# Kernel tuning notes

Measured on AMD Instinct MI355X. Metric: run time of the kernel, lower is better.

Reference implementation:

```python
import jax, jax.numpy as jnp
import numpy as np

H = 256    # hidden_size
NH = 8     # num_heads
B = 256    # batch_size (num graphs)
M = 128    # max_num_nodes per graph
N = B * M  # total nodes
E = N * 16 # total edges


def _bn(x, g, b, eps=1e-5):
    # BatchNorm1d in training mode: batch stats over node dim, biased variance
    m = x.mean(0)
    v = ((x - m) ** 2).mean(0)
    return g * (x - m) * jax.lax.rsqrt(v + eps) + b


def setup_inputs() -> dict:
    key = jax.random.key(0)
    ks = jax.random.split(key, 12)
    def lin(k, o, i):
        return jax.random.normal(k, (o, i), jnp.float32) / np.sqrt(i).astype(np.float32)
    return {
        "h": jax.random.normal(ks[0], (N, H), jnp.float32),
        "gin_w1": lin(ks[1], H, H), "gin_b1": jnp.zeros((H,), jnp.float32),
        "gin_w2": lin(ks[2], H, H), "gin_b2": jnp.zeros((H,), jnp.float32),
        "in_proj_w": lin(ks[3], 3 * H, H), "in_proj_b": jnp.zeros((3 * H,), jnp.float32),
        "out_proj_w": lin(ks[4], H, H), "out_proj_b": jnp.zeros((H,), jnp.float32),
        "bn_local_g": jnp.ones((H,), jnp.float32), "bn_local_b": jnp.zeros((H,), jnp.float32),
        "bn_attn_g": jnp.ones((H,), jnp.float32), "bn_attn_b": jnp.zeros((H,), jnp.float32),
        "bn_out_g": jnp.ones((H,), jnp.float32), "bn_out_b": jnp.zeros((H,), jnp.float32),
        "ffn1_w": lin(ks[5], 2 * H, H), "ffn1_b": jnp.zeros((2 * H,), jnp.float32),
        "ffn2_w": lin(ks[6], H, 2 * H), "ffn2_b": jnp.zeros((H,), jnp.float32),
        "edge_src": jax.random.randint(ks[7], (E,), 0, N, dtype=jnp.int32),
        "edge_dst": jax.random.randint(ks[8], (E,), 0, N, dtype=jnp.int32),
        "batch_num_nodes": jnp.full((B,), M, dtype=jnp.int32),
    }


def reference(h, gin_w1, gin_b1, gin_w2, gin_b2, in_proj_w, in_proj_b,
              out_proj_w, out_proj_b, bn_local_g, bn_local_b, bn_attn_g, bn_attn_b,
              bn_out_g, bn_out_b, ffn1_w, ffn1_b, ffn2_w, ffn2_b,
              edge_src, edge_dst, batch_num_nodes):
    # ---- local GIN conv: gin_nn((1+eps)*h + sum_neighbors h), eps=0 ----
    agg = jax.ops.segment_sum(h[edge_src], edge_dst, num_segments=N)
    z = h + agg
    z = jax.nn.relu(z @ gin_w1.T + gin_b1) @ gin_w2.T + gin_b2
    h_local = _bn(h + z, bn_local_g, bn_local_b)  # dropout=0

    # ---- to_dense_batch scatter indices ----
    cum = jnp.concatenate([jnp.zeros((1,), batch_num_nodes.dtype), jnp.cumsum(batch_num_nodes)])
    node = jnp.arange(N, dtype=jnp.int32)
    bid = jnp.searchsorted(cum[1:], node, side='right')  # graph id per node
    idx = node - cum[bid] + bid * M                      # slot in dense [B*M]
    hd = jnp.zeros((B * M, H), h.dtype).at[idx].set(h).reshape(B, M, H)
    mask = jnp.zeros((B * M,), bool).at[idx].set(True).reshape(B, M)

    # ---- MultiheadAttention (batch_first, self-attn, key_padding_mask) ----
    qkv = hd @ in_proj_w.T + in_proj_b
    q, k, v = jnp.split(qkv, 3, axis=-1)
    dh = H // NH
    q = q.reshape(B, M, NH, dh)
    k = k.reshape(B, M, NH, dh)
    v = v.reshape(B, M, NH, dh)
    scores = jnp.einsum('bqhd,bkhd->bhqk', q, k) / np.float32(np.sqrt(dh))
    scores = jnp.where(mask[:, None, None, :], scores, jnp.float32(-1e9))
    attn = jax.nn.softmax(scores, axis=-1)
    ao = jnp.einsum('bhqk,bkhd->bqhd', attn, v).reshape(B, M, H)
    ao = ao @ out_proj_w.T + out_proj_b
    h_attn = ao.reshape(B * M, H)[idx]  # ragged gather back (x[mask])
    h_attn = _bn(h + h_attn, bn_attn_g, bn_attn_b)

    # ---- combine + FFN + out norm ----
    hh = h_local + h_attn
    hh = hh + (jax.nn.relu(hh @ ffn1_w.T + ffn1_b) @ ffn2_w.T + ffn2_b)
    return _bn(hh, bn_out_g, bn_out_b)
```

## Files before the change

kernel.cpp:

```cpp
#include <hip/hip_runtime.h>

#define NNODES 32768
#define HDIM   256
#define NHEADS 8
#define NB     256
#define NEDGES 524288


typedef unsigned short u16;
typedef unsigned int   u32;
typedef __attribute__((ext_vector_type(8))) short short8;
typedef __attribute__((ext_vector_type(4))) float f32x4;

__device__ __forceinline__ float bf2f(u16 u){
  union { u32 i; float f; } x; x.i = ((u32)u) << 16; return x.f;
}
__device__ __forceinline__ u16 f2bf(float f){
  union { float f; u32 i; } x; x.f = f;
  u32 r = x.i + 0x7fffu + ((x.i >> 16) & 1u);
  return (u16)(r >> 16);
}
__device__ __forceinline__ void unpack8(uint4 v, float* f){
  f[0] = bf2f((u16)(v.x & 0xffff)); f[1] = bf2f((u16)(v.x >> 16));
  f[2] = bf2f((u16)(v.y & 0xffff)); f[3] = bf2f((u16)(v.y >> 16));
  f[4] = bf2f((u16)(v.z & 0xffff)); f[5] = bf2f((u16)(v.z >> 16));
  f[6] = bf2f((u16)(v.w & 0xffff)); f[7] = bf2f((u16)(v.w >> 16));
}
__device__ __forceinline__ uint4 pack8(const float* f){
  uint4 v;
  v.x = (u32)f2bf(f[0]) | ((u32)f2bf(f[1]) << 16);
  v.y = (u32)f2bf(f[2]) | ((u32)f2bf(f[3]) << 16);
  v.z = (u32)f2bf(f[4]) | ((u32)f2bf(f[5]) << 16);
  v.w = (u32)f2bf(f[6]) | ((u32)f2bf(f[7]) << 16);
  return v;
}

struct CvtPtrs { const void* p[19]; };

__device__ static const int CVT_CH[19] = {
  2097152,16384,64,16384,64,49152,192,16384,64,64,64,64,64,64,64,32768,128,32768,64};
__device__ static const int CVT_PR[19] = {
  0,8388608,8454144,8454400,8519936,8520192,8716800,8717568,8783104,
  8783360,8783616,8783872,8784128,8784384,8784640,8784896,8915968,8916480,9047552};
#define CVT_TOTAL_CHUNKS 2261952

__global__ __launch_bounds__(256) void convert_k(CvtPtrs cp, u16* __restrict__ dst){
  int gid = blockIdx.x * 256 + threadIdx.x;
  if (gid >= CVT_TOTAL_CHUNKS) return;
  int t = 0, rem = gid;
  while (t < 18 && rem >= CVT_CH[t]) { rem -= CVT_CH[t]; t++; }
  u16* d = dst + CVT_PR[t] + (size_t)rem * 4;
  float4 v = ((const float4*)cp.p[t])[rem];
  u16 o[4] = { f2bf(v.x), f2bf(v.y), f2bf(v.z), f2bf(v.w) };
  *(uint2*)d = *(const uint2*)o;
}

__global__ void count_k(const int* __restrict__ dst, int* __restrict__ counts){
  int e = blockIdx.x * 256 + threadIdx.x;
  atomicAdd(&counts[dst[e]], 1);
}

__global__ void scan_k(const int* __restrict__ counts, int* __restrict__ offsets,
                       int* __restrict__ cursor){
  __shared__ int part[1024];
  int t = threadIdx.x;
  int local[32];
  int s = 0;
  int base = t * 32;
#pragma unroll
  for (int i = 0; i < 32; i++){ local[i] = counts[base + i]; s += local[i]; }
  part[t] = s;
  __syncthreads();
  for (int off = 1; off < 1024; off <<= 1){
    int v = (t >= off) ? part[t - off] : 0;
    __syncthreads();
    part[t] += v;
    __syncthreads();
  }
  int run = part[t] - s;
#pragma unroll
  for (int i = 0; i < 32; i++){
    offsets[base + i] = run; cursor[base + i] = run; run += local[i];
  }
  if (t == 1023) offsets[NNODES] = run;
}

__global__ void bucket_k(const int* __restrict__ src, const int* __restrict__ dst,
                         int* __restrict__ cursor, int* __restrict__ srcs){
  int e = blockIdx.x * 256 + threadIdx.x;
  int p = atomicAdd(&cursor[dst[e]], 1);
  srcs[p] = src[e];
}

__global__ __launch_bounds__(256) void agg_k(const u16* __restrict__ h,
    const int* __restrict__ offsets, const int* __restrict__ srcs,
    u16* __restrict__ z0){
  int node = blockIdx.x * 4 + (threadIdx.x >> 6);
  int lane = threadIdx.x & 63;
  size_t coff = (size_t)lane * 4;
  int beg = offsets[node], end = offsets[node + 1];

  uint2 self = *(const uint2*)&h[(size_t)node * HDIM + coff];
  float a0 = bf2f((u16)(self.x & 0xffff)), a1 = bf2f((u16)(self.x >> 16));
  float a2 = bf2f((u16)(self.y & 0xffff)), a3 = bf2f((u16)(self.y >> 16));

  int e = beg;
  for (; e + 8 <= end; e += 8){
    uint2 v[8];
#pragma unroll
    for (int i = 0; i < 8; i++){
      int s = srcs[e + i];
      v[i] = *(const uint2*)&h[(size_t)s * HDIM + coff];
    }
#pragma unroll
    for (int i = 0; i < 8; i++){
      a0 += bf2f((u16)(v[i].x & 0xffff));
      a1 += bf2f((u16)(v[i].x >> 16));
      a2 += bf2f((u16)(v[i].y & 0xffff));
      a3 += bf2f((u16)(v[i].y >> 16));
    }
  }
  for (; e < end; e++){
    int s = srcs[e];
    uint2 va = *(const uint2*)&h[(size_t)s * HDIM + coff];
    a0 += bf2f((u16)(va.x & 0xffff));
    a1 += bf2f((u16)(va.x >> 16));
    a2 += bf2f((u16)(va.y & 0xffff));
    a3 += bf2f((u16)(va.y >> 16));
  }

  uint2 o;
  o.x = (u32)f2bf(a0) | ((u32)f2bf(a1) << 16);
  o.y = (u32)f2bf(a2) | ((u32)f2bf(a3) << 16);
  *(uint2*)&z0[(size_t)node * HDIM + coff] = o;
}

template<int NO, int K, bool RELU, bool RES, bool STATS>
__global__ __launch_bounds__(256) void gemm_bt(const u16* __restrict__ A,
    const u16* __restrict__ W, const u16* __restrict__ bias,
    const u16* __restrict__ res, u16* __restrict__ C,
    float* __restrict__ ssum, float* __restrict__ ssq){
  __shared__ u16 As[128 * 40];
  __shared__ u16 Ws[128 * 40];
  const int tid = threadIdx.x;
  const int m0 = blockIdx.y * 128;
  const int n0 = blockIdx.x * 128;
  const int wave = tid >> 6, lane = tid & 63;
  const int wm = wave >> 1, wn = wave & 1;
  const int q4 = lane >> 4, ln = lane & 15;

  f32x4 acc[4][4] = {};

  const int r_a = tid >> 2;
  const int c_a = tid & 3;

  for (int k0 = 0; k0 < K; k0 += 32){
    uint4 a0 = *(const uint4*)&A[(size_t)(m0 + r_a) * K + k0 + c_a * 8];
    uint4 a1 = *(const uint4*)&A[(size_t)(m0 + r_a + 64) * K + k0 + c_a * 8];
    uint4 w0 = *(const uint4*)&W[(size_t)(n0 + r_a) * K + k0 + c_a * 8];
    uint4 w1 = *(const uint4*)&W[(size_t)(n0 + r_a + 64) * K + k0 + c_a * 8];
    __syncthreads();
    *(uint4*)&As[r_a * 40 + c_a * 8] = a0;
    *(uint4*)&As[(r_a + 64) * 40 + c_a * 8] = a1;
    *(uint4*)&Ws[r_a * 40 + c_a * 8] = w0;
    *(uint4*)&Ws[(r_a + 64) * 40 + c_a * 8] = w1;
    __syncthreads();

    short8 af[4], bfr[4];
#pragma unroll
    for (int mt = 0; mt < 4; mt++)
      af[mt] = *(const short8*)&As[(wm * 64 + mt * 16 + ln) * 40 + q4 * 8];
#pragma unroll
    for (int nt = 0; nt < 4; nt++)
      bfr[nt] = *(const short8*)&Ws[(wn * 64 + nt * 16 + ln) * 40 + q4 * 8];
#pragma unroll
    for (int mt = 0; mt < 4; mt++)
#pragma unroll
      for (int nt = 0; nt < 4; nt++)
        acc[mt][nt] = __builtin_amdgcn_mfma_f32_16x16x32_bf16(af[mt], bfr[nt], acc[mt][nt], 0, 0, 0);
  }

#pragma unroll
  for (int nt = 0; nt < 4; nt++){
    int col = n0 + wn * 64 + nt * 16 + ln;
    float bv = bf2f(bias[col]);
    float cs = 0.0f, cq = 0.0f;
#pragma unroll
    for (int mt = 0; mt < 4; mt++){
      int row = m0 + wm * 64 + mt * 16 + q4 * 4;
#pragma unroll
      for (int reg = 0; reg < 4; reg++){
        float v = acc[mt][nt][reg] + bv;
        if (RELU) v = fmaxf(v, 0.0f);
        if (RES)  v += bf2f(res[(size_t)(row + reg) * NO + col]);
        C[(size_t)(row + reg) * NO + col] = f2bf(v);
        if (STATS){ cs += v; cq += v * v; }
      }
    }
    if (STATS){
      cs += __shfl_xor(cs, 16); cs += __shfl_xor(cs, 32);
      cq += __shfl_xor(cq, 16); cq += __shfl_xor(cq, 32);
      if (lane < 16){
        atomicAdd(&ssum[col], cs);
        atomicAdd(&ssq[col], cq);
      }
    }
  }
}

__global__ __launch_bounds__(256) void attn_k(const u16* __restrict__ qkv,
                                              u16* __restrict__ ao){
  __shared__ u16 Qs[128 * 40];
  __shared__ u16 Ks[128 * 40];
  __shared__ u16 VTs[32 * 136];
  __shared__ u16 Ps[128 * 136];

  const int b  = blockIdx.x >> 3;
  const int nh = blockIdx.x & 7;
  const int tid = threadIdx.x;
  const int wave = tid >> 6, lane = tid & 63;
  const int q4 = lane >> 4, ln = lane & 15;

#pragma unroll
  for (int c2 = 0; c2 < 2; c2++){
    int chunk = tid + c2 * 256;
    int r = chunk >> 2;
    int cc = chunk & 3;
    size_t nb = (size_t)(b * 128 + r) * 768 + nh * 32 + cc * 8;
    uint4 vq = *(const uint4*)&qkv[nb];
    uint4 vk = *(const uint4*)&qkv[nb + 256];
    uint4 vv = *(const uint4*)&qkv[nb + 512];
    *(uint4*)&Qs[r * 40 + cc * 8] = vq;
    *(uint4*)&Ks[r * 40 + cc * 8] = vk;
    union { uint4 v; u16 h[8]; } uv; uv.v = vv;
#pragma unroll
    for (int i = 0; i < 8; i++) VTs[(cc * 8 + i) * 136 + r] = uv.h[i];
  }
  __syncthreads();

  f32x4 accs[2][8] = {};
  short8 qf[2];
#pragma unroll
  for (int mt = 0; mt < 2; mt++)
    qf[mt] = *(const short8*)&Qs[(wave * 32 + mt * 16 + ln) * 40 + q4 * 8];
#pragma unroll
  for (int nt = 0; nt < 8; nt++){
    short8 kf = *(const short8*)&Ks[(nt * 16 + ln) * 40 + q4 * 8];
    accs[0][nt] = __builtin_amdgcn_mfma_f32_16x16x32_bf16(qf[0], kf, accs[0][nt], 0, 0, 0);
    accs[1][nt] = __builtin_amdgcn_mfma_f32_16x16x32_bf16(qf[1], kf, accs[1][nt], 0, 0, 0);
  }

  const float scale = 0.17677669529663687f;
  float invs[2][4];
#pragma unroll
  for (int mt = 0; mt < 2; mt++){
#pragma unroll
    for (int reg = 0; reg < 4; reg++){
      float rm = -1e30f;
#pragma unroll
      for (int nt = 0; nt < 8; nt++){
        accs[mt][nt][reg] *= scale;
        rm = fmaxf(rm, accs[mt][nt][reg]);
      }
      for (int m = 1; m < 16; m <<= 1) rm = fmaxf(rm, __shfl_xor(rm, m));
      float rs = 0.0f;
#pragma unroll
      for (int nt = 0; nt < 8; nt++){
        float e = __expf(accs[mt][nt][reg] - rm);
        accs[mt][nt][reg] = e;
        rs += e;
      }
      for (int m = 1; m < 16; m <<= 1) rs += __shfl_xor(rs, m);
      invs[mt][reg] = 1.0f / rs;
    }
  }

#pragma unroll
  for (int mt = 0; mt < 2; mt++)
#pragma unroll
    for (int nt = 0; nt < 8; nt++)
#pragma unroll
      for (int reg = 0; reg < 4; reg++)
        Ps[(wave * 32 + mt * 16 + q4 * 4 + reg) * 136 + nt * 16 + ln] =
            f2bf(accs[mt][nt][reg] * invs[mt][reg]);
  __syncthreads();

  f32x4 acco[2][2] = {};
#pragma unroll
  for (int kk = 0; kk < 4; kk++){
    short8 pf[2], vf[2];
#pragma unroll
    for (int mt = 0; mt < 2; mt++)
      pf[mt] = *(const short8*)&Ps[(wave * 32 + mt * 16 + ln) * 136 + kk * 32 + q4 * 8];
#pragma unroll
    for (int nt = 0; nt < 2; nt++)
      vf[nt] = *(const short8*)&VTs[(nt * 16 + ln) * 136 + kk * 32 + q4 * 8];
#pragma unroll
    for (int mt = 0; mt < 2; mt++)
#pragma unroll
      for (int nt = 0; nt < 2; nt++)
        acco[mt][nt] = __builtin_amdgcn_mfma_f32_16x16x32_bf16(pf[mt], vf[nt], acco[mt][nt], 0, 0, 0);
  }

#pragma unroll
  for (int mt = 0; mt < 2; mt++)
#pragma unroll
    for (int nt = 0; nt < 2; nt++)
#pragma unroll
      for (int reg = 0; reg < 4; reg++){
        int node = b * 128 + wave * 32 + mt * 16 + q4 * 4 + reg;
        int col = nh * 32 + nt * 16 + ln;
        ao[(size_t)node * HDIM + col] = f2bf(acco[mt][nt][reg]);
      }
}

__global__ void bncoef2_k(const float* __restrict__ stats,
    const u16* __restrict__ gl, const u16* __restrict__ bl,
    const u16* __restrict__ ga, const u16* __restrict__ ba,
    float* __restrict__ coef){
  int c = threadIdx.x;
  const float invN = 1.0f / 32768.0f;
  float mA = stats[c] * invN;
  float vA = stats[256 + c] * invN - mA * mA;
  float sA = bf2f(gl[c]) * rsqrtf(vA + 1e-5f);
  float tA = bf2f(bl[c]) - mA * sA;
  float mB = stats[512 + c] * invN;
  float vB = stats[768 + c] * invN - mB * mB;
  float sB = bf2f(ga[c]) * rsqrtf(vB + 1e-5f);
  float tB = bf2f(ba[c]) - mB * sB;
  coef[c] = sA; coef[256 + c] = sB; coef[512 + c] = tA + tB;
}

__global__ void bncoef1_k(const float* __restrict__ stats,
    const u16* __restrict__ g, const u16* __restrict__ bb,
    float* __restrict__ coef){
  int c = threadIdx.x;
  const float invN = 1.0f / 32768.0f;
  float m = stats[1024 + c] * invN;
  float v = stats[1280 + c] * invN - m * m;
  float s = bf2f(g[c]) * rsqrtf(v + 1e-5f);
  coef[768 + c] = s; coef[1024 + c] = bf2f(bb[c]) - m * s;
}

__global__ __launch_bounds__(256) void combine_k(const u16* __restrict__ xl,
    const u16* __restrict__ xa, const float* __restrict__ coef,
    u16* __restrict__ hh){
  int gid = blockIdx.x * 256 + threadIdx.x;
  size_t off = (size_t)gid * 8;
  int cb = (int)(off & 255);
  float sl[8], sa[8], tt[8];
  *(float4*)&sl[0] = *(const float4*)&coef[cb];
  *(float4*)&sl[4] = *(const float4*)&coef[cb + 4];
  *(float4*)&sa[0] = *(const float4*)&coef[256 + cb];
  *(float4*)&sa[4] = *(const float4*)&coef[256 + cb + 4];
  *(float4*)&tt[0] = *(const float4*)&coef[512 + cb];
  *(float4*)&tt[4] = *(const float4*)&coef[512 + cb + 4];
  float fl[8], fa[8], fo[8];
  unpack8(*(const uint4*)&xl[off], fl);
  unpack8(*(const uint4*)&xa[off], fa);
#pragma unroll
  for (int i = 0; i < 8; i++) fo[i] = sl[i] * fl[i] + sa[i] * fa[i] + tt[i];
  *(uint4*)&hh[off] = pack8(fo);
}

__global__ __launch_bounds__(256) void finalbn_k(const u16* __restrict__ y,
    const float* __restrict__ coef, float* __restrict__ out){
  int gid = blockIdx.x * 256 + threadIdx.x;
  size_t off = (size_t)gid * 8;
  int cb = (int)(off & 255);
  float ss[8], tt[8];
  *(float4*)&ss[0] = *(const float4*)&coef[768 + cb];
  *(float4*)&ss[4] = *(const float4*)&coef[768 + cb + 4];
  *(float4*)&tt[0] = *(const float4*)&coef[1024 + cb];
  *(float4*)&tt[4] = *(const float4*)&coef[1024 + cb + 4];
  float fy[8], fo[8];
  unpack8(*(const uint4*)&y[off], fy);
#pragma unroll
  for (int i = 0; i < 8; i++) fo[i] = ss[i] * fy[i] + tt[i];
  *(float4*)&out[off] = *(const float4*)&fo[0];
  *(float4*)&out[off + 4] = *(const float4*)&fo[4];
}

extern "C" void kernel_launch(void* const* d_in, const int* in_sizes, int n_in,
                              void* d_out, int out_size, void* d_ws, size_t ws_size,
                              hipStream_t stream){
  const int* edge_src = (const int*)d_in[19];
  const int* edge_dst = (const int*)d_in[20];

  char* ws = (char*)d_ws;
  float* stats = (float*)ws;
  float* coef  = (float*)(ws + 6144);
  u16*   conv  = (u16*)(ws + 12288);
  u16*   A     = (u16*)(ws + 12288 + 18095616);
  u16*   B     = (u16*)(ws + 12288 + 18095616 + 16777216);
  u16*   C     = (u16*)d_out;
  int* counts  = (int*)B;
  int* offsets = (int*)((char*)B + 131072);
  int* cursor  = (int*)((char*)B + 262400);
  int* srcs    = (int*)((char*)B + 393472);

  const u16* convH = conv;
  const u16* W1  = conv + 8388608; const u16* b1g = conv + 8454144;
  const u16* W2  = conv + 8454400; const u16* b2g = conv + 8519936;
  const u16* Win = conv + 8520192; const u16* bin = conv + 8716800;
  const u16* Wo  = conv + 8717568; const u16* bo  = conv + 8783104;
  const u16* g_l = conv + 8783360; const u16* b_l = conv + 8783616;
  const u16* g_a = conv + 8783872; const u16* b_a = conv + 8784128;
  const u16* g_o = conv + 8784384; const u16* b_o = conv + 8784640;
  const u16* Wf1 = conv + 8784896; const u16* bf1 = conv + 8915968;
  const u16* Wf2 = conv + 8916480; const u16* bf2 = conv + 9047552;

  hipMemsetAsync(ws, 0, 12288, stream);
  hipMemsetAsync(counts, 0, 131072, stream);

  CvtPtrs cp;
  for (int i = 0; i < 19; i++) cp.p[i] = d_in[i];
  convert_k<<<8836, 256, 0, stream>>>(cp, conv);

  count_k<<<NEDGES / 256, 256, 0, stream>>>(edge_dst, counts);
  scan_k<<<1, 1024, 0, stream>>>(counts, offsets, cursor);
  bucket_k<<<NEDGES / 256, 256, 0, stream>>>(edge_src, edge_dst, cursor, srcs);
  agg_k<<<NNODES / 4, 256, 0, stream>>>(convH, offsets, srcs, A);

  gemm_bt<256, 256, true,  false, false><<<dim3(2, 256), 256, 0, stream>>>(
      A, W1, b1g, nullptr, B, nullptr, nullptr);
  gemm_bt<256, 256, false, true,  true ><<<dim3(2, 256), 256, 0, stream>>>(
      B, W2, b2g, convH, A, stats + 0, stats + 256);

  for (int c = 0; c < 4; c++){
    const u16* hA = convH + (size_t)c * 8192 * HDIM;
    u16* aoC = C + (size_t)c * 8192 * HDIM;
    gemm_bt<768, 256, false, false, false><<<dim3(6, 64), 256, 0, stream>>>(
        hA, Win, bin, nullptr, B, nullptr, nullptr);
    attn_k<<<512, 256, 0, stream>>>(B, aoC);
  }

  gemm_bt<256, 256, false, true, true><<<dim3(2, 256), 256, 0, stream>>>(
      C, Wo, bo, convH, B, stats + 512, stats + 768);

  bncoef2_k<<<1, 256, 0, stream>>>(stats, g_l, b_l, g_a, b_a, coef);
  combine_k<<<4096, 256, 0, stream>>>(A, B, coef, C);

  gemm_bt<512, 256, true,  false, false><<<dim3(4, 256), 256, 0, stream>>>(
      C, Wf1, bf1, nullptr, A, nullptr, nullptr);
  gemm_bt<256, 512, false, true,  true ><<<dim3(2, 256), 256, 0, stream>>>(
      A, Wf2, bf2, C, (u16*)conv, stats + 1024, stats + 1280);

  bncoef1_k<<<1, 256, 0, stream>>>(stats, g_o, b_o, coef);
  finalbn_k<<<4096, 256, 0, stream>>>(conv, coef, (float*)d_out);
}
```

Measured before the change: 457.9 us.

## Double-buffer GEMM via direct global-to-LDS loads and fold small kernels into neighbours

The GEMM now double-buffers its tiles in LDS, filled with global_load_lds direct copies, so the next K-slice loads while MFMAs run on the current one. The edge counting is fused into the convert kernel, and the BN coefficient kernels are folded into the combine and final-BN kernels, which removes several launches. When the workspace is large enough, the QKV projection and attention run as one full-size launch each instead of four chunks. The risks are LDS bank conflicts from the unpadded 32-stride layout, and every combine/finalbn block now recomputes the BN coefficients.

```diff
diff --git a/kernel.cpp b/kernel.cpp
--- a/kernel.cpp
+++ b/kernel.cpp
@@ -9,6 +9,7 @@
 
 typedef unsigned short u16;
 typedef unsigned int   u32;
+typedef unsigned long long u64;
 typedef __attribute__((ext_vector_type(8))) short short8;
 typedef __attribute__((ext_vector_type(4))) float f32x4;
 
@@ -35,6 +36,13 @@
   return v;
 }
 
+typedef __attribute__((address_space(3))) unsigned int lds_u32;
+typedef const __attribute__((address_space(1))) unsigned int gbl_u32;
+__device__ __forceinline__ void gload16(const void* g, void* l){
+  __builtin_amdgcn_global_load_lds((gbl_u32*)(u64)g,
+                                   (lds_u32*)(u32)(u64)l, 16, 0, 0);
+}
+
 struct CvtPtrs { const void* p[19]; };
 
 __device__ static const int CVT_CH[19] = {
@@ -44,8 +52,10 @@
   8783360,8783616,8783872,8784128,8784384,8784640,8784896,8915968,8916480,9047552};
 #define CVT_TOTAL_CHUNKS 2261952
 
-__global__ __launch_bounds__(256) void convert_k(CvtPtrs cp, u16* __restrict__ dst){
+__global__ __launch_bounds__(256) void convert_k(CvtPtrs cp, u16* __restrict__ dst,
+    const int* __restrict__ edge_dst, int* __restrict__ counts){
   int gid = blockIdx.x * 256 + threadIdx.x;
+  if (gid < NEDGES) atomicAdd(&counts[edge_dst[gid]], 1);
   if (gid >= CVT_TOTAL_CHUNKS) return;
   int t = 0, rem = gid;
   while (t < 18 && rem >= CVT_CH[t]) { rem -= CVT_CH[t]; t++; }
@@ -55,11 +65,6 @@
   *(uint2*)d = *(const uint2*)o;
 }
 
-__global__ void count_k(const int* __restrict__ dst, int* __restrict__ counts){
-  int e = blockIdx.x * 256 + threadIdx.x;
-  atomicAdd(&counts[dst[e]], 1);
-}
-
 __global__ void scan_k(const int* __restrict__ counts, int* __restrict__ offsets,
                        int* __restrict__ cursor){
   __shared__ int part[1024];
@@ -135,13 +140,28 @@
   *(uint2*)&z0[(size_t)node * HDIM + coff] = o;
 }
 
+__device__ __forceinline__ void mfma_step(const u16* AS_, const u16* WS_,
+    f32x4 (&acc)[4][4], int wm, int wn, int ln, int q4){
+  short8 af[4], bfr[4];
+#pragma unroll
+  for (int mt = 0; mt < 4; mt++)
+    af[mt] = *(const short8*)&AS_[(wm * 64 + mt * 16 + ln) * 32 + q4 * 8];
+#pragma unroll
+  for (int nt = 0; nt < 4; nt++)
+    bfr[nt] = *(const short8*)&WS_[(wn * 64 + nt * 16 + ln) * 32 + q4 * 8];
+#pragma unroll
+  for (int mt = 0; mt < 4; mt++)
+#pragma unroll
+    for (int nt = 0; nt < 4; nt++)
+      acc[mt][nt] = __builtin_amdgcn_mfma_f32_16x16x32_bf16(af[mt], bfr[nt], acc[mt][nt], 0, 0, 0);
+}
+
 template<int NO, int K, bool RELU, bool RES, bool STATS>
 __global__ __launch_bounds__(256) void gemm_bt(const u16* __restrict__ A,
     const u16* __restrict__ W, const u16* __restrict__ bias,
     const u16* __restrict__ res, u16* __restrict__ C,
     float* __restrict__ ssum, float* __restrict__ ssq){
-  __shared__ u16 As[128 * 40];
-  __shared__ u16 Ws[128 * 40];
+  __shared__ u16 As0[4096], Ws0[4096], As1[4096], Ws1[4096];
   const int tid = threadIdx.x;
   const int m0 = blockIdx.y * 128;
   const int n0 = blockIdx.x * 128;
@@ -151,33 +171,35 @@
 
   f32x4 acc[4][4] = {};
 
-  const int r_a = tid >> 2;
-  const int c_a = tid & 3;
-
-  for (int k0 = 0; k0 < K; k0 += 32){
-    uint4 a0 = *(const uint4*)&A[(size_t)(m0 + r_a) * K + k0 + c_a * 8];
-    uint4 a1 = *(const uint4*)&A[(size_t)(m0 + r_a + 64) * K + k0 + c_a * 8];
-    uint4 w0 = *(const uint4*)&W[(size_t)(n0 + r_a) * K + k0 + c_a * 8];
-    uint4 w1 = *(const uint4*)&W[(size_t)(n0 + r_a + 64) * K + k0 + c_a * 8];
+  const int r_l = tid >> 2;
+  const int c_l = (tid & 3) * 8;
+  const u16* gA = A + (size_t)(m0 + r_l) * K + c_l;
+  const u16* gW = W + (size_t)(n0 + r_l) * K + c_l;
+  u16* dA0 = As0 + wave * 512; u16* dW0 = Ws0 + wave * 512;
+  u16* dA1 = As1 + wave * 512; u16* dW1 = Ws1 + wave * 512;
+
+  const int NT = K / 32;
+
+  gload16(gA, dA0); gload16(gA + 64 * K, dA0 + 2048);
+  gload16(gW, dW0); gload16(gW + 64 * K, dW0 + 2048);
+  __syncthreads();
+
+#pragma unroll
+  for (int t = 0; t < NT; t += 2){
+    if (t + 1 < NT){
+      int kn = (t + 1) * 32;
+      gload16(gA + kn, dA1); gload16(gA + 64 * K + kn, dA1 + 2048);
+      gload16(gW + kn, dW1); gload16(gW + 64 * K + kn, dW1 + 2048);
+    }
+    mfma_step(As0, Ws0, acc, wm, wn, ln, q4);
     __syncthreads();
-    *(uint4*)&As[r_a * 40 + c_a * 8] = a0;
-    *(uint4*)&As[(r_a + 64) * 40 + c_a * 8] = a1;
-    *(uint4*)&Ws[r_a * 40 + c_a * 8] = w0;
-    *(uint4*)&Ws[(r_a + 64) * 40 + c_a * 8] = w1;
+    if (t + 2 < NT){
+      int kn = (t + 2) * 32;
+      gload16(gA + kn, dA0); gload16(gA + 64 * K + kn, dA0 + 2048);
+      gload16(gW + kn, dW0); gload16(gW + 64 * K + kn, dW0 + 2048);
+    }
+    mfma_step(As1, Ws1, acc, wm, wn, ln, q4);
     __syncthreads();
-
-    short8 af[4], bfr[4];
-#pragma unroll
-    for (int mt = 0; mt < 4; mt++)
-      af[mt] = *(const short8*)&As[(wm * 64 + mt * 16 + ln) * 40 + q4 * 8];
-#pragma unroll
-    for (int nt = 0; nt < 4; nt++)
-      bfr[nt] = *(const short8*)&Ws[(wn * 64 + nt * 16 + ln) * 40 + q4 * 8];
-#pragma unroll
-    for (int mt = 0; mt < 4; mt++)
-#pragma unroll
-      for (int nt = 0; nt < 4; nt++)
-        acc[mt][nt] = __builtin_amdgcn_mfma_f32_16x16x32_bf16(af[mt], bfr[nt], acc[mt][nt], 0, 0, 0);
   }
 
 #pragma unroll
@@ -314,47 +336,36 @@
       }
 }
 
-__global__ void bncoef2_k(const float* __restrict__ stats,
+__global__ __launch_bounds__(256) void combine_k(const u16* __restrict__ xl,
+    const u16* __restrict__ xa, const float* __restrict__ stats,
     const u16* __restrict__ gl, const u16* __restrict__ bl,
     const u16* __restrict__ ga, const u16* __restrict__ ba,
-    float* __restrict__ coef){
-  int c = threadIdx.x;
-  const float invN = 1.0f / 32768.0f;
-  float mA = stats[c] * invN;
-  float vA = stats[256 + c] * invN - mA * mA;
-  float sA = bf2f(gl[c]) * rsqrtf(vA + 1e-5f);
-  float tA = bf2f(bl[c]) - mA * sA;
-  float mB = stats[512 + c] * invN;
-  float vB = stats[768 + c] * invN - mB * mB;
-  float sB = bf2f(ga[c]) * rsqrtf(vB + 1e-5f);
-  float tB = bf2f(ba[c]) - mB * sB;
-  coef[c] = sA; coef[256 + c] = sB; coef[512 + c] = tA + tB;
-}
-
-__global__ void bncoef1_k(const float* __restrict__ stats,
-    const u16* __restrict__ g, const u16* __restrict__ bb,
-    float* __restrict__ coef){
-  int c = threadIdx.x;
-  const float invN = 1.0f / 32768.0f;
-  float m = stats[1024 + c] * invN;
-  float v = stats[1280 + c] * invN - m * m;
-  float s = bf2f(g[c]) * rsqrtf(v + 1e-5f);
-  coef[768 + c] = s; coef[1024 + c] = bf2f(bb[c]) - m * s;
-}
-
-__global__ __launch_bounds__(256) void combine_k(const u16* __restrict__ xl,
-    const u16* __restrict__ xa, const float* __restrict__ coef,
     u16* __restrict__ hh){
-  int gid = blockIdx.x * 256 + threadIdx.x;
+  __shared__ float cs0[256], cs1[256], cs2[256];
+  int t = threadIdx.x;
+  {
+    const float invN = 1.0f / 32768.0f;
+    float mA = stats[t] * invN;
+    float vA = stats[256 + t] * invN - mA * mA;
+    float sA = bf2f(gl[t]) * rsqrtf(vA + 1e-5f);
+    float tA = bf2f(bl[t]) - mA * sA;
+    float mB = stats[512 + t] * invN;
+    float vB = stats[768 + t] * invN - mB * mB;
+    float sB = bf2f(ga[t]) * rsqrtf(vB + 1e-5f);
+    float tB = bf2f(ba[t]) - mB * sB;
+    cs0[t] = sA; cs1[t] = sB; cs2[t] = tA + tB;
+  }
+  __syncthreads();
+  int gid = blockIdx.x * 256 + t;
   size_t off = (size_t)gid * 8;
   int cb = (int)(off & 255);
   float sl[8], sa[8], tt[8];
-  *(float4*)&sl[0] = *(const float4*)&coef[cb];
-  *(float4*)&sl[4] = *(const float4*)&coef[cb + 4];
-  *(float4*)&sa[0] = *(const float4*)&coef[256 + cb];
-  *(float4*)&sa[4] = *(const float4*)&coef[256 + cb + 4];
-  *(float4*)&tt[0] = *(const float4*)&coef[512 + cb];
-  *(float4*)&tt[4] = *(const float4*)&coef[512 + cb + 4];
+  *(float4*)&sl[0] = *(const float4*)&cs0[cb];
+  *(float4*)&sl[4] = *(const float4*)&cs0[cb + 4];
+  *(float4*)&sa[0] = *(const float4*)&cs1[cb];
+  *(float4*)&sa[4] = *(const float4*)&cs1[cb + 4];
+  *(float4*)&tt[0] = *(const float4*)&cs2[cb];
+  *(float4*)&tt[4] = *(const float4*)&cs2[cb + 4];
   float fl[8], fa[8], fo[8];
   unpack8(*(const uint4*)&xl[off], fl);
   unpack8(*(const uint4*)&xa[off], fa);
@@ -364,15 +375,26 @@
 }
 
 __global__ __launch_bounds__(256) void finalbn_k(const u16* __restrict__ y,
-    const float* __restrict__ coef, float* __restrict__ out){
-  int gid = blockIdx.x * 256 + threadIdx.x;
+    const float* __restrict__ stats, const u16* __restrict__ g,
+    const u16* __restrict__ bb, float* __restrict__ out){
+  __shared__ float cs0[256], cs1[256];
+  int t = threadIdx.x;
+  {
+    const float invN = 1.0f / 32768.0f;
+    float m = stats[1024 + t] * invN;
+    float v = stats[1280 + t] * invN - m * m;
+    float s = bf2f(g[t]) * rsqrtf(v + 1e-5f);
+    cs0[t] = s; cs1[t] = bf2f(bb[t]) - m * s;
+  }
+  __syncthreads();
+  int gid = blockIdx.x * 256 + t;
   size_t off = (size_t)gid * 8;
   int cb = (int)(off & 255);
   float ss[8], tt[8];
-  *(float4*)&ss[0] = *(const float4*)&coef[768 + cb];
-  *(float4*)&ss[4] = *(const float4*)&coef[768 + cb + 4];
-  *(float4*)&tt[0] = *(const float4*)&coef[1024 + cb];
-  *(float4*)&tt[4] = *(const float4*)&coef[1024 + cb + 4];
+  *(float4*)&ss[0] = *(const float4*)&cs0[cb];
+  *(float4*)&ss[4] = *(const float4*)&cs0[cb + 4];
+  *(float4*)&tt[0] = *(const float4*)&cs1[cb];
+  *(float4*)&tt[4] = *(const float4*)&cs1[cb + 4];
   float fy[8], fo[8];
   unpack8(*(const uint4*)&y[off], fy);
 #pragma unroll
@@ -389,11 +411,14 @@
 
   char* ws = (char*)d_ws;
   float* stats = (float*)ws;
-  float* coef  = (float*)(ws + 6144);
   u16*   conv  = (u16*)(ws + 12288);
   u16*   A     = (u16*)(ws + 12288 + 18095616);
   u16*   B     = (u16*)(ws + 12288 + 18095616 + 16777216);
   u16*   C     = (u16*)d_out;
+  const size_t BIG_NEED = 51662336ull + 50331648ull;
+  const bool big = (ws_size >= BIG_NEED);
+  u16* QKV = (u16*)(ws + 51662336);
+
   int* counts  = (int*)B;
   int* offsets = (int*)((char*)B + 131072);
   int* cursor  = (int*)((char*)B + 262400);
@@ -410,14 +435,13 @@
   const u16* Wf1 = conv + 8784896; const u16* bf1 = conv + 8915968;
   const u16* Wf2 = conv + 8916480; const u16* bf2 = conv + 9047552;
 
-  hipMemsetAsync(ws, 0, 12288, stream);
+  hipMemsetAsync(ws, 0, 6144, stream);
   hipMemsetAsync(counts, 0, 131072, stream);
 
   CvtPtrs cp;
   for (int i = 0; i < 19; i++) cp.p[i] = d_in[i];
-  convert_k<<<8836, 256, 0, stream>>>(cp, conv);
-
-  count_k<<<NEDGES / 256, 256, 0, stream>>>(edge_dst, counts);
+  convert_k<<<8836, 256, 0, stream>>>(cp, conv, edge_dst, counts);
+
   scan_k<<<1, 1024, 0, stream>>>(counts, offsets, cursor);
   bucket_k<<<NEDGES / 256, 256, 0, stream>>>(edge_src, edge_dst, cursor, srcs);
   agg_k<<<NNODES / 4, 256, 0, stream>>>(convH, offsets, srcs, A);
@@ -427,25 +451,29 @@
   gemm_bt<256, 256, false, true,  true ><<<dim3(2, 256), 256, 0, stream>>>(
       B, W2, b2g, convH, A, stats + 0, stats + 256);
 
-  for (int c = 0; c < 4; c++){
-    const u16* hA = convH + (size_t)c * 8192 * HDIM;
-    u16* aoC = C + (size_t)c * 8192 * HDIM;
-    gemm_bt<768, 256, false, false, false><<<dim3(6, 64), 256, 0, stream>>>(
-        hA, Win, bin, nullptr, B, nullptr, nullptr);
-    attn_k<<<512, 256, 0, stream>>>(B, aoC);
+  if (big){
+    gemm_bt<768, 256, false, false, false><<<dim3(6, 256), 256, 0, stream>>>(
+        convH, Win, bin, nullptr, QKV, nullptr, nullptr);
+    attn_k<<<2048, 256, 0, stream>>>(QKV, C);
+  } else {
+    for (int c = 0; c < 4; c++){
+      const u16* hA = convH + (size_t)c * 8192 * HDIM;
+      u16* aoC = C + (size_t)c * 8192 * HDIM;
+      gemm_bt<768, 256, false, false, false><<<dim3(6, 64), 256, 0, stream>>>(
+          hA, Win, bin, nullptr, B, nullptr, nullptr);
+      attn_k<<<512, 256, 0, stream>>>(B, aoC);
+    }
   }
 
   gemm_bt<256, 256, false, true, true><<<dim3(2, 256), 256, 0, stream>>>(
       C, Wo, bo, convH, B, stats + 512, stats + 768);
 
-  bncoef2_k<<<1, 256, 0, stream>>>(stats, g_l, b_l, g_a, b_a, coef);
-  combine_k<<<4096, 256, 0, stream>>>(A, B, coef, C);
+  combine_k<<<4096, 256, 0, stream>>>(A, B, stats, g_l, b_l, g_a, b_a, C);
 
   gemm_bt<512, 256, true,  false, false><<<dim3(4, 256), 256, 0, stream>>>(
       C, Wf1, bf1, nullptr, A, nullptr, nullptr);
   gemm_bt<256, 512, false, true,  true ><<<dim3(2, 256), 256, 0, stream>>>(
       A, Wf2, bf2, C, (u16*)conv, stats + 1024, stats + 1280);
 
-  bncoef1_k<<<1, 256, 0, stream>>>(stats, g_o, b_o, coef);
-  finalbn_k<<<4096, 256, 0, stream>>>(conv, coef, (float*)d_out);
-}
+  finalbn_k<<<4096, 256, 0, stream>>>(conv, stats, g_o, b_o, (float*)d_out);
+}
```

Result: faster. 424.6 us (-7.3%).
